# Kernel tuning notes

Hardware: AMD Instinct MI355X
Metric: run time of the kernel (lower is better)

The kernel has to match this reference:

```python
import jax, jax.numpy as jnp
import numpy as np

N_NODES = 100000
N_EDGES = 1600000
IN_CH, HID_CH, OUT_CH = 128, 256, 128


def _sage_conv(x, src, dst, W_l, b_l, W_r, n_nodes):
    """PyG SAGEConv with mean aggregation: lin_l(mean_j x_j) + lin_r(x)."""
    # gather source features per edge, scatter-sum into destination nodes
    agg = jax.ops.segment_sum(x[src], dst, num_segments=n_nodes)  # [N, C]
    deg = jax.ops.segment_sum(jnp.ones((src.shape[0],), x.dtype), dst,
                              num_segments=n_nodes)               # [N]
    mean = agg / jnp.maximum(deg, 1.0)[:, None]
    return mean @ W_l + b_l + x @ W_r


def setup_inputs() -> dict:
    key = jax.random.key(0)
    ks = jax.random.split(key, 8)
    x = jax.random.normal(ks[0], (N_NODES, IN_CH), dtype=jnp.float32)
    edge_index = jax.random.randint(ks[1], (2, N_EDGES), 0, N_NODES, dtype=jnp.int64)
    s1 = 1.0 / np.sqrt(IN_CH)
    s2 = 1.0 / np.sqrt(HID_CH)
    W1_l = jax.random.normal(ks[2], (IN_CH, HID_CH), dtype=jnp.float32) * s1
    W1_r = jax.random.normal(ks[3], (IN_CH, HID_CH), dtype=jnp.float32) * s1
    b1 = jnp.zeros((HID_CH,), dtype=jnp.float32)
    W2_l = jax.random.normal(ks[4], (HID_CH, OUT_CH), dtype=jnp.float32) * s2
    W2_r = jax.random.normal(ks[5], (HID_CH, OUT_CH), dtype=jnp.float32) * s2
    b2 = jnp.zeros((OUT_CH,), dtype=jnp.float32)
    return {"x": x, "edge_index": edge_index, "W1_l": W1_l, "b1": b1,
            "W1_r": W1_r, "W2_l": W2_l, "b2": b2, "W2_r": W2_r}


def reference(x, edge_index, W1_l, b1, W1_r, W2_l, b2, W2_r):
    src, dst = edge_index[0], edge_index[1]
    h = _sage_conv(x, src, dst, W1_l, b1, W1_r, N_NODES)
    h = jax.nn.relu(h)
    out = _sage_conv(h, src, dst, W2_l, b2, W2_r, N_NODES)
    return out
```

## Files before the change

kernel.cpp:

```cpp
#include <hip/hip_runtime.h>
#include <cstddef>

#define N_NODES_C 100000
#define N_EDGES_C 1600000

#define NPB 64
#define NB 1563
#define BCAP 1408
#define SENT_ROW 100000

#define CONV_BLOCKS 12500
#define WB_BLOCKS 512
#define P1_BLOCKS 1563

typedef unsigned short u16;
typedef __attribute__((ext_vector_type(8))) short bf16x8;
typedef __attribute__((ext_vector_type(4))) float f32x4;

__device__ __forceinline__ u16 f2bf(float f) {
    unsigned u = __float_as_uint(f);
    u += 0x7fffu + ((u >> 16) & 1);
    return (u16)(u >> 16);
}
__device__ __forceinline__ float lo16f(unsigned v) {
    return __uint_as_float(v << 16);
}
__device__ __forceinline__ float hi16f(unsigned v) {
    return __uint_as_float(v & 0xffff0000u);
}


__global__ __launch_bounds__(256) void front_fused(
    const float* __restrict__ x, const int* __restrict__ dst,
    const float* __restrict__ W1l, const float* __restrict__ W1r,
    const float* __restrict__ W2l, const float* __restrict__ W2r,
    u16* __restrict__ x_bf, u16* __restrict__ T1l, u16* __restrict__ T1r,
    u16* __restrict__ T2l, u16* __restrict__ T2r,
    int* __restrict__ bucket_counts, u16* __restrict__ p2z) {
    const int b = blockIdx.x;
    const int t = threadIdx.x;
    if (b < CONV_BLOCKS) {
        int i = b * 256 + t;
        if (i < 3200000) {
            float4 v = ((const float4*)x)[i];
            ushort4 o;
            o.x = f2bf(v.x); o.y = f2bf(v.y); o.z = f2bf(v.z); o.w = f2bf(v.w);
            ((ushort4*)x_bf)[i] = o;
        }
    } else if (b < CONV_BLOCKS + WB_BLOCKS) {
        int id = (b - CONV_BLOCKS) * 256 + t;
        int which = id >> 15;
        int r = id & 32767;
        if (which == 0) {
            int n = r >> 7, k = r & 127;
            T1l[r] = f2bf(W1l[k * 256 + n]);
        } else if (which == 1) {
            int n = r >> 7, k = r & 127;
            T1r[r] = f2bf(W1r[k * 256 + n]);
        } else if (which == 2) {
            int n = r >> 8, k = r & 255;
            T2l[r] = f2bf(W2l[k * 128 + n]);
        } else {
            int n = r >> 8, k = r & 255;
            T2r[r] = f2bf(W2r[k * 128 + n]);
        }
    } else if (b < CONV_BLOCKS + WB_BLOCKS + P1_BLOCKS) {
        __shared__ int hist[NB];
        for (int j = t; j < NB; j += 256) hist[j] = 0;
        __syncthreads();
        int i = (b - CONV_BLOCKS - WB_BLOCKS) * 256 + t;
        if (i * 4 < N_EDGES_C) {
            int4 d = ((const int4*)dst)[i];
            atomicAdd(&hist[d.x >> 6], 1);
            atomicAdd(&hist[d.y >> 6], 1);
            atomicAdd(&hist[d.z >> 6], 1);
            atomicAdd(&hist[d.w >> 6], 1);
        }
        __syncthreads();
        for (int j = t; j < NB; j += 256) {
            int c = hist[j];
            if (c) atomicAdd(&bucket_counts[j], c);
        }
    } else {
        uint4 z; z.x = 0; z.y = 0; z.z = 0; z.w = 0;
        if (t < 16)
            ((uint4*)(x_bf + (size_t)SENT_ROW * 128))[t] = z;
        else if (t < 32)
            ((uint4*)(p2z + (size_t)SENT_ROW * 128))[t - 16] = z;
    }
}


__global__ __launch_bounds__(1024) void bucket_scan(const int* __restrict__ counts,
                                                    int* __restrict__ base,
                                                    int* __restrict__ cursor) {
    __shared__ int s[1024];
    int t = threadIdx.x;
    int c0 = counts[2 * t];
    int c1 = counts[2 * t + 1];
    int v = c0 + c1;
    s[t] = v;
    __syncthreads();
    for (int off = 1; off < 1024; off <<= 1) {
        int u = (t >= off) ? s[t - off] : 0;
        __syncthreads();
        s[t] += u;
        __syncthreads();
    }
    int excl = s[t] - v;
    base[2 * t] = excl;
    cursor[2 * t] = excl;
    base[2 * t + 1] = excl + c0;
    cursor[2 * t + 1] = excl + c0;
}


__global__ __launch_bounds__(1024) void p2_scatter(const int* __restrict__ src,
                                                   const int* __restrict__ dst,
                                                   int* __restrict__ cursor,
                                                   unsigned* __restrict__ edge_pkt) {
    __shared__ int hist[NB];
    __shared__ int lbase[NB];
    __shared__ int cur2[NB];
    int t = threadIdx.x;
    for (int j = t; j < NB; j += 1024) { hist[j] = 0; cur2[j] = 0; }
    __syncthreads();

    int4 dd[4];
    int idx[4];
#pragma unroll
    for (int r = 0; r < 4; ++r) {
        int i = blockIdx.x * 4096 + r * 1024 + t;
        idx[r] = i;
        if (i * 4 < N_EDGES_C) {
            int4 d = ((const int4*)dst)[i];
            dd[r] = d;
            atomicAdd(&hist[d.x >> 6], 1);
            atomicAdd(&hist[d.y >> 6], 1);
            atomicAdd(&hist[d.z >> 6], 1);
            atomicAdd(&hist[d.w >> 6], 1);
        }
    }
    __syncthreads();
    for (int j = t; j < NB; j += 1024) {
        int c = hist[j];
        if (c) lbase[j] = atomicAdd(&cursor[j], c);
    }
    __syncthreads();

#pragma unroll
    for (int r = 0; r < 4; ++r) {
        int i = idx[r];
        if (i * 4 < N_EDGES_C) {
            int4 s4 = ((const int4*)src)[i];
            int4 d = dd[r];
            {
                int bk = d.x >> 6, local = d.x & 63;
                int pos = lbase[bk] + atomicAdd(&cur2[bk], 1);
                edge_pkt[pos] = ((unsigned)local << 17) | (unsigned)s4.x;
            }
            {
                int bk = d.y >> 6, local = d.y & 63;
                int pos = lbase[bk] + atomicAdd(&cur2[bk], 1);
                edge_pkt[pos] = ((unsigned)local << 17) | (unsigned)s4.y;
            }
            {
                int bk = d.z >> 6, local = d.z & 63;
                int pos = lbase[bk] + atomicAdd(&cur2[bk], 1);
                edge_pkt[pos] = ((unsigned)local << 17) | (unsigned)s4.z;
            }
            {
                int bk = d.w >> 6, local = d.w & 63;
                int pos = lbase[bk] + atomicAdd(&cur2[bk], 1);
                edge_pkt[pos] = ((unsigned)local << 17) | (unsigned)s4.w;
            }
        }
    }
}


__global__ __launch_bounds__(256, 2) void fused_gemm_agg(
    const u16* __restrict__ x_bf,
    const int* __restrict__ base, const unsigned* __restrict__ edge_pkt,
    const u16* __restrict__ T1l, const u16* __restrict__ T1r,
    const u16* __restrict__ T2l, const u16* __restrict__ T2r,
    const float* __restrict__ b1, const float* __restrict__ b2,
    u16* __restrict__ p2, u16* __restrict__ outp, int M) {
    alignas(16) __shared__ u16 uni[64 * 256];
    alignas(16) __shared__ u16 Bs[8192];
    __shared__ unsigned se[BCAP];
    __shared__ int lhist[64];
    __shared__ int lstart[64];
    __shared__ int lcur[64];
    __shared__ int stmp[64];

    u16* const meanS = uni;
    u16* const xS = uni + 64 * 128;
    u16* const hfrag = uni;

    const int tid = threadIdx.x;
    const int lane = tid & 63;
    const int wave = tid >> 6;
    const int qm = lane & 15;
    const int quad = lane >> 4;
    const int b = blockIdx.x;
    const int m0 = b * 64;

#pragma unroll
    for (int r = 0; r < 4; ++r) {
        int c = r * 256 + tid;
        int row = c >> 4, q16 = c & 15;
        __builtin_amdgcn_global_load_lds(
            (const __attribute__((address_space(1))) unsigned*)(
                x_bf + (size_t)(m0 + row) * 128 + ((q16 ^ (row & 7)) * 8)),
            (__attribute__((address_space(3))) unsigned*)(xS + c * 8), 16, 0, 0);
    }

    if (tid < 64) lhist[tid] = 0;
    __syncthreads();

    const int ebeg = base[b];
    int ecnt = base[b + 1] - ebeg;
    if (ecnt > BCAP) ecnt = BCAP;

    for (int i = tid; i < ecnt; i += 256)
        atomicAdd(&lhist[edge_pkt[ebeg + i] >> 17], 1);
    __syncthreads();

    if (tid < 64) stmp[tid] = lhist[tid];
    __syncthreads();
    for (int off = 1; off < 64; off <<= 1) {
        int v = 0;
        if (tid < 64 && tid >= off) v = stmp[tid - off];
        __syncthreads();
        if (tid < 64) stmp[tid] += v;
        __syncthreads();
    }
    if (tid < 64) {
        int excl = stmp[tid] - lhist[tid];
        lstart[tid] = excl;
        lcur[tid] = excl;
    }
    __syncthreads();

    for (int i = tid; i < ecnt; i += 256) {
        unsigned p = edge_pkt[ebeg + i];
        int pos = atomicAdd(&lcur[p >> 17], 1);
        se[pos] = p & 0x1ffffu;
    }
    __syncthreads();

    const int g = quad;
    const int li16 = qm;
    const int li8 = li16 * 8;

    for (int pass = 0; pass < 4; ++pass) {
        int n = pass * 16 + wave * 4 + g;
        int d = lhist[n];
        int s0 = lstart[n];
        int dmax = max(d, __shfl_xor(d, 16, 64));
        dmax = max(dmax, __shfl_xor(dmax, 32, 64));

        float a0 = 0.f, a1 = 0.f, a2 = 0.f, a3 = 0.f;
        float a4 = 0.f, a5 = 0.f, a6 = 0.f, a7 = 0.f;

        for (int j = 0; j < dmax; j += 4) {
            unsigned ix[4];
#pragma unroll
            for (int u = 0; u < 4; ++u) {
                int jj = j + u;
                int sa = s0 + jj;
                if (sa > BCAP - 1) sa = BCAP - 1;
                unsigned sv = se[sa];
                ix[u] = (jj < d) ? sv : (unsigned)SENT_ROW;
            }
            uint4 r0 = *(const uint4*)(x_bf + (size_t)ix[0] * 128 + li8);
            uint4 r1 = *(const uint4*)(x_bf + (size_t)ix[1] * 128 + li8);
            uint4 r2 = *(const uint4*)(x_bf + (size_t)ix[2] * 128 + li8);
            uint4 r3 = *(const uint4*)(x_bf + (size_t)ix[3] * 128 + li8);

            a0 += lo16f(r0.x); a1 += hi16f(r0.x);
            a2 += lo16f(r0.y); a3 += hi16f(r0.y);
            a4 += lo16f(r0.z); a5 += hi16f(r0.z);
            a6 += lo16f(r0.w); a7 += hi16f(r0.w);
            a0 += lo16f(r1.x); a1 += hi16f(r1.x);
            a2 += lo16f(r1.y); a3 += hi16f(r1.y);
            a4 += lo16f(r1.z); a5 += hi16f(r1.z);
            a6 += lo16f(r1.w); a7 += hi16f(r1.w);
            a0 += lo16f(r2.x); a1 += hi16f(r2.x);
            a2 += lo16f(r2.y); a3 += hi16f(r2.y);
            a4 += lo16f(r2.z); a5 += hi16f(r2.z);
            a6 += lo16f(r2.w); a7 += hi16f(r2.w);
            a0 += lo16f(r3.x); a1 += hi16f(r3.x);
            a2 += lo16f(r3.y); a3 += hi16f(r3.y);
            a4 += lo16f(r3.z); a5 += hi16f(r3.z);
            a6 += lo16f(r3.w); a7 += hi16f(r3.w);
        }

        float inv = d > 0 ? 1.f / (float)d : 0.f;
        uint4 o;
        o.x = (unsigned)f2bf(a0 * inv) | ((unsigned)f2bf(a1 * inv) << 16);
        o.y = (unsigned)f2bf(a2 * inv) | ((unsigned)f2bf(a3 * inv) << 16);
        o.z = (unsigned)f2bf(a4 * inv) | ((unsigned)f2bf(a5 * inv) << 16);
        o.w = (unsigned)f2bf(a6 * inv) | ((unsigned)f2bf(a7 * inv) << 16);
        *(uint4*)(meanS + n * 128 + ((li16 ^ (n & 7)) * 8)) = o;
    }
    __syncthreads();

    const int wr0 = (wave >> 1) * 32;
    const int wc0 = (wave & 1) * 128;
    f32x4 acch[2][8];
#pragma unroll
    for (int i = 0; i < 2; ++i)
#pragma unroll
        for (int j = 0; j < 8; ++j) acch[i][j] = (f32x4){0.f, 0.f, 0.f, 0.f};

#pragma unroll
    for (int mat = 0; mat < 2; ++mat) {
        const u16* __restrict__ W = mat ? T1r : T1l;
        const u16* Al = mat ? xS : meanS;
#pragma unroll
        for (int k0 = 0; k0 < 128; k0 += 32) {
#pragma unroll
            for (int r = 0; r < 4; ++r) {
                int c = r * 256 + tid;
                int row = c >> 2, kc = c & 3;
                __builtin_amdgcn_global_load_lds(
                    (const __attribute__((address_space(1))) unsigned*)(
                        W + (size_t)row * 128 + k0 + ((kc ^ (row & 3)) * 8)),
                    (__attribute__((address_space(3))) unsigned*)(Bs + c * 8), 16, 0, 0);
            }
            __syncthreads();
            int ch0 = k0 >> 3;
            bf16x8 af[2], bfv[8];
#pragma unroll
            for (int i = 0; i < 2; ++i) {
                int row = wr0 + i * 16 + qm;
                af[i] = *(const bf16x8*)(Al + row * 128 +
                                         (((ch0 + quad) ^ (row & 7)) * 8));
            }
#pragma unroll
            for (int j = 0; j < 8; ++j) {
                int rB = wc0 + j * 16 + qm;
                bfv[j] = *(const bf16x8*)(Bs + rB * 32 + ((quad ^ (rB & 3)) * 8));
            }
#pragma unroll
            for (int i = 0; i < 2; ++i)
#pragma unroll
                for (int j = 0; j < 8; ++j)
                    acch[i][j] = __builtin_amdgcn_mfma_f32_16x16x32_bf16(
                        af[i], bfv[j], acch[i][j], 0, 0, 0);
            __syncthreads();
        }
    }

#pragma unroll
    for (int j = 0; j < 8; ++j) {
        int n = wc0 + j * 16 + qm;
        float bb = b1[n];
        int ks = n >> 5, quadB = (n >> 3) & 3, jB = n & 7;
#pragma unroll
        for (int i = 0; i < 2; ++i) {
#pragma unroll
            for (int r = 0; r < 4; ++r) {
                int mloc = wr0 + i * 16 + quad * 4 + r;
                float v = fmaxf(acch[i][j][r] + bb, 0.f);
                hfrag[((ks * 4 + (mloc >> 4)) * 16 + (mloc & 15)) * 32 + quadB * 8 + jB] =
                    f2bf(v);
            }
        }
    }
    __syncthreads();

    const int wrB = (wave >> 1) * 32;
    const int wcB = (wave & 1) * 64;
    f32x4 accp[2][4], acco[2][4];
#pragma unroll
    for (int i = 0; i < 2; ++i)
#pragma unroll
        for (int j = 0; j < 4; ++j) {
            accp[i][j] = (f32x4){0.f, 0.f, 0.f, 0.f};
            acco[i][j] = (f32x4){0.f, 0.f, 0.f, 0.f};
        }

#pragma unroll
    for (int ks = 0; ks < 8; ++ks) {
#pragma unroll
        for (int r = 0; r < 4; ++r) {
            int c = r * 256 + tid;
            int matc = c >> 9;
            int row = (c >> 2) & 127;
            int kc = c & 3;
            const u16* W = matc ? T2r : T2l;
            __builtin_amdgcn_global_load_lds(
                (const __attribute__((address_space(1))) unsigned*)(
                    W + (size_t)row * 256 + ks * 32 + ((kc ^ (row & 3)) * 8)),
                (__attribute__((address_space(3))) unsigned*)(Bs + c * 8), 16, 0, 0);
        }
        __syncthreads();
        bf16x8 af[2], bfl[4], bfr[4];
#pragma unroll
        for (int i = 0; i < 2; ++i)
            af[i] = *(const bf16x8*)(hfrag +
                                     ((ks * 4 + (wrB >> 4) + i) * 16 + qm) * 32 + quad * 8);
#pragma unroll
        for (int j = 0; j < 4; ++j) {
            int rB = wcB + j * 16 + qm;
            bfl[j] = *(const bf16x8*)(Bs + rB * 32 + ((quad ^ (rB & 3)) * 8));
            bfr[j] = *(const bf16x8*)(Bs + 4096 + rB * 32 + ((quad ^ (rB & 3)) * 8));
        }
#pragma unroll
        for (int i = 0; i < 2; ++i)
#pragma unroll
            for (int j = 0; j < 4; ++j) {
                accp[i][j] = __builtin_amdgcn_mfma_f32_16x16x32_bf16(af[i], bfl[j],
                                                                    accp[i][j], 0, 0, 0);
                acco[i][j] = __builtin_amdgcn_mfma_f32_16x16x32_bf16(af[i], bfr[j],
                                                                    acco[i][j], 0, 0, 0);
            }
        __syncthreads();
    }

#pragma unroll
    for (int j = 0; j < 4; ++j) {
        int n = wcB + j * 16 + qm;
        float bb2 = b2[n];
#pragma unroll
        for (int i = 0; i < 2; ++i) {
#pragma unroll
            for (int r = 0; r < 4; ++r) {
                int row = m0 + wrB + i * 16 + quad * 4 + r;
                if (row < M) {
                    p2[(size_t)row * 128 + n] = f2bf(accp[i][j][r]);
                    outp[(size_t)row * 128 + n] = f2bf(acco[i][j][r] + bb2);
                }
            }
        }
    }
}


__global__ __launch_bounds__(256, 8) void agg_final(const u16* __restrict__ tbl,
                                                    const int* __restrict__ base,
                                                    const unsigned* __restrict__ edge_pkt,
                                                    const u16* __restrict__ resid,
                                                    float* __restrict__ outv) {
    __shared__ unsigned se[BCAP];
    __shared__ int lhist[64];
    __shared__ int lstart[64];
    __shared__ int lcur[64];
    __shared__ int stmp[64];

    const int t = threadIdx.x;
    const int wave = t >> 6;
    const int lane = t & 63;
    const int b = blockIdx.x;

    if (t < 64) lhist[t] = 0;
    __syncthreads();

    const int ebeg = base[b];
    int ecnt = base[b + 1] - ebeg;
    if (ecnt > BCAP) ecnt = BCAP;

    for (int i = t; i < ecnt; i += 256)
        atomicAdd(&lhist[edge_pkt[ebeg + i] >> 17], 1);
    __syncthreads();

    if (t < 64) stmp[t] = lhist[t];
    __syncthreads();
    for (int off = 1; off < 64; off <<= 1) {
        int v = 0;
        if (t < 64 && t >= off) v = stmp[t - off];
        __syncthreads();
        if (t < 64) stmp[t] += v;
        __syncthreads();
    }
    if (t < 64) {
        int excl = stmp[t] - lhist[t];
        lstart[t] = excl;
        lcur[t] = excl;
    }
    __syncthreads();

    for (int i = t; i < ecnt; i += 256) {
        unsigned p = edge_pkt[ebeg + i];
        int pos = atomicAdd(&lcur[p >> 17], 1);
        se[pos] = p & 0x1ffffu;
    }
    __syncthreads();

    const int g = lane >> 4;
    const int li8 = (lane & 15) * 8;

    for (int pass = 0; pass < 4; ++pass) {
        int n = pass * 16 + wave * 4 + g;
        int node = b * NPB + n;
        bool valid = node < N_NODES_C;
        int d = 0, s0 = 0;
        if (valid) { d = lhist[n]; s0 = lstart[n]; }
        int dmax = max(d, __shfl_xor(d, 16, 64));
        dmax = max(dmax, __shfl_xor(dmax, 32, 64));

        float a0 = 0.f, a1 = 0.f, a2 = 0.f, a3 = 0.f;
        float a4 = 0.f, a5 = 0.f, a6 = 0.f, a7 = 0.f;

        for (int j = 0; j < dmax; j += 4) {
            unsigned ix[4];
#pragma unroll
            for (int u = 0; u < 4; ++u) {
                int jj = j + u;
                int sa = s0 + jj;
                if (sa > BCAP - 1) sa = BCAP - 1;
                unsigned sv = se[sa];
                ix[u] = (jj < d) ? sv : (unsigned)SENT_ROW;
            }
            uint4 r0 = *(const uint4*)(tbl + (size_t)ix[0] * 128 + li8);
            uint4 r1 = *(const uint4*)(tbl + (size_t)ix[1] * 128 + li8);
            uint4 r2 = *(const uint4*)(tbl + (size_t)ix[2] * 128 + li8);
            uint4 r3 = *(const uint4*)(tbl + (size_t)ix[3] * 128 + li8);

            a0 += lo16f(r0.x); a1 += hi16f(r0.x);
            a2 += lo16f(r0.y); a3 += hi16f(r0.y);
            a4 += lo16f(r0.z); a5 += hi16f(r0.z);
            a6 += lo16f(r0.w); a7 += hi16f(r0.w);
            a0 += lo16f(r1.x); a1 += hi16f(r1.x);
            a2 += lo16f(r1.y); a3 += hi16f(r1.y);
            a4 += lo16f(r1.z); a5 += hi16f(r1.z);
            a6 += lo16f(r1.w); a7 += hi16f(r1.w);
            a0 += lo16f(r2.x); a1 += hi16f(r2.x);
            a2 += lo16f(r2.y); a3 += hi16f(r2.y);
            a4 += lo16f(r2.z); a5 += hi16f(r2.z);
            a6 += lo16f(r2.w); a7 += hi16f(r2.w);
            a0 += lo16f(r3.x); a1 += hi16f(r3.x);
            a2 += lo16f(r3.y); a3 += hi16f(r3.y);
            a4 += lo16f(r3.z); a5 += hi16f(r3.z);
            a6 += lo16f(r3.w); a7 += hi16f(r3.w);
        }

        if (valid) {
            float inv = d > 0 ? 1.f / (float)d : 0.f;
            uint4 rp = *(const uint4*)(resid + (size_t)node * 128 + li8);
            float* op = outv + (size_t)node * 128 + li8;
            float4 o0, o1;
            o0.x = a0 * inv + lo16f(rp.x);
            o0.y = a1 * inv + hi16f(rp.x);
            o0.z = a2 * inv + lo16f(rp.y);
            o0.w = a3 * inv + hi16f(rp.y);
            o1.x = a4 * inv + lo16f(rp.z);
            o1.y = a5 * inv + hi16f(rp.z);
            o1.z = a6 * inv + lo16f(rp.w);
            o1.w = a7 * inv + hi16f(rp.w);
            *(float4*)op = o0;
            *(float4*)(op + 4) = o1;
        }
    }
}


extern "C" void kernel_launch(void* const* d_in, const int* in_sizes, int n_in,
                              void* d_out, int out_size, void* d_ws, size_t ws_size,
                              hipStream_t stream) {
    const float* x = (const float*)d_in[0];
    const int* ei = (const int*)d_in[1];
    const float* W1l = (const float*)d_in[2];
    const float* b1 = (const float*)d_in[3];
    const float* W1r = (const float*)d_in[4];
    const float* W2l = (const float*)d_in[5];
    const float* b2 = (const float*)d_in[6];
    const float* W2r = (const float*)d_in[7];
    float* out = (float*)d_out;

    const int* src = ei;
    const int* dst = ei + N_EDGES_C;

    int* iw = (int*)d_ws;
    int* bucket_counts = iw;
    int* bucket_base = iw + 2048;
    int* cursor = iw + 4096;
    unsigned* edge_pkt = (unsigned*)(iw + 6144);
    u16* T1l = (u16*)(iw + 1606144);
    u16* T1r = T1l + 32768;
    u16* T2l = T1r + 32768;
    u16* T2r = T2l + 32768;
    u16* ub = (u16*)((char*)d_ws + (8u << 20));
    u16* x_bf = ub;
    u16* p2 = ub + 12850000;
    u16* outp = ub + 25700000;

    hipMemsetAsync(bucket_counts, 0, 2048 * sizeof(int), stream);

    front_fused<<<CONV_BLOCKS + WB_BLOCKS + P1_BLOCKS + 1, 256, 0, stream>>>(
        x, dst, W1l, W1r, W2l, W2r, x_bf, T1l, T1r, T2l, T2r, bucket_counts, p2);
    bucket_scan<<<1, 1024, 0, stream>>>(bucket_counts, bucket_base, cursor);
    p2_scatter<<<(N_EDGES_C / 4 + 4095) / 4096, 1024, 0, stream>>>(src, dst, cursor,
                                                                   edge_pkt);

    fused_gemm_agg<<<NB, 256, 0, stream>>>(x_bf, bucket_base, edge_pkt, T1l, T1r,
                                           T2l, T2r, b1, b2, p2, outp, N_NODES_C);
    agg_final<<<NB, 256, 0, stream>>>(p2, bucket_base, edge_pkt, outp, out);
}
```

Baseline: 396.9 us.

## Build per-node CSR with global atomics and drop per-block LDS edge sort

Replaces the bucketed edge packing and in-kernel LDS counting sort with a per-node degree histogram, a multi-block scan with atomic offset allocation, and direct per-node scatter of source indices. The aggregation loops read indices from global memory, coalesced per 16 lanes, and broadcast them with shuffles. The fused GEMM kernel is widened to 512 threads with smaller per-wave tiles. This removes LDS sort and barrier overhead and the edge-capacity cap, at the price of many more contended global atomics in the degree and scatter passes.

```diff
diff --git a/kernel.cpp b/kernel.cpp
--- a/kernel.cpp
+++ b/kernel.cpp
@@ -6,12 +6,11 @@
 
 #define NPB 64
 #define NB 1563
-#define BCAP 1408
 #define SENT_ROW 100000
 
 #define CONV_BLOCKS 12500
 #define WB_BLOCKS 512
-#define P1_BLOCKS 1563
+#define DEG_BLOCKS 1563
 
 typedef unsigned short u16;
 typedef __attribute__((ext_vector_type(8))) short bf16x8;
@@ -36,7 +35,7 @@
     const float* __restrict__ W2l, const float* __restrict__ W2r,
     u16* __restrict__ x_bf, u16* __restrict__ T1l, u16* __restrict__ T1r,
     u16* __restrict__ T2l, u16* __restrict__ T2r,
-    int* __restrict__ bucket_counts, u16* __restrict__ p2z) {
+    int* __restrict__ deg, u16* __restrict__ p2z) {
     const int b = blockIdx.x;
     const int t = threadIdx.x;
     if (b < CONV_BLOCKS) {
@@ -64,22 +63,14 @@
             int n = r >> 8, k = r & 255;
             T2r[r] = f2bf(W2r[k * 128 + n]);
         }
-    } else if (b < CONV_BLOCKS + WB_BLOCKS + P1_BLOCKS) {
-        __shared__ int hist[NB];
-        for (int j = t; j < NB; j += 256) hist[j] = 0;
-        __syncthreads();
+    } else if (b < CONV_BLOCKS + WB_BLOCKS + DEG_BLOCKS) {
         int i = (b - CONV_BLOCKS - WB_BLOCKS) * 256 + t;
         if (i * 4 < N_EDGES_C) {
             int4 d = ((const int4*)dst)[i];
-            atomicAdd(&hist[d.x >> 6], 1);
-            atomicAdd(&hist[d.y >> 6], 1);
-            atomicAdd(&hist[d.z >> 6], 1);
-            atomicAdd(&hist[d.w >> 6], 1);
-        }
-        __syncthreads();
-        for (int j = t; j < NB; j += 256) {
-            int c = hist[j];
-            if (c) atomicAdd(&bucket_counts[j], c);
+            atomicAdd(&deg[d.x], 1);
+            atomicAdd(&deg[d.y], 1);
+            atomicAdd(&deg[d.z], 1);
+            atomicAdd(&deg[d.w], 1);
         }
     } else {
         uint4 z; z.x = 0; z.y = 0; z.z = 0; z.w = 0;
@@ -91,14 +82,15 @@
 }
 
 
-__global__ __launch_bounds__(1024) void bucket_scan(const int* __restrict__ counts,
-                                                    int* __restrict__ base,
-                                                    int* __restrict__ cursor) {
+__global__ __launch_bounds__(1024) void scan_alloc(const int* __restrict__ deg,
+                                                   int* __restrict__ gctr,
+                                                   int* __restrict__ base,
+                                                   int* __restrict__ cursor) {
     __shared__ int s[1024];
+    __shared__ int sofs;
     int t = threadIdx.x;
-    int c0 = counts[2 * t];
-    int c1 = counts[2 * t + 1];
-    int v = c0 + c1;
+    int i = blockIdx.x * 1024 + t;
+    int v = (i < N_NODES_C) ? deg[i] : 0;
     s[t] = v;
     __syncthreads();
     for (int off = 1; off < 1024; off <<= 1) {
@@ -107,92 +99,41 @@
         s[t] += u;
         __syncthreads();
     }
-    int excl = s[t] - v;
-    base[2 * t] = excl;
-    cursor[2 * t] = excl;
-    base[2 * t + 1] = excl + c0;
-    cursor[2 * t + 1] = excl + c0;
+    if (t == 1023) sofs = atomicAdd(gctr, s[1023]);
+    __syncthreads();
+    if (i < N_NODES_C) {
+        int e = sofs + s[t] - v;
+        base[i] = e;
+        cursor[i] = e;
+    }
 }
 
 
 __global__ __launch_bounds__(1024) void p2_scatter(const int* __restrict__ src,
                                                    const int* __restrict__ dst,
                                                    int* __restrict__ cursor,
-                                                   unsigned* __restrict__ edge_pkt) {
-    __shared__ int hist[NB];
-    __shared__ int lbase[NB];
-    __shared__ int cur2[NB];
-    int t = threadIdx.x;
-    for (int j = t; j < NB; j += 1024) { hist[j] = 0; cur2[j] = 0; }
-    __syncthreads();
-
-    int4 dd[4];
-    int idx[4];
-#pragma unroll
-    for (int r = 0; r < 4; ++r) {
-        int i = blockIdx.x * 4096 + r * 1024 + t;
-        idx[r] = i;
-        if (i * 4 < N_EDGES_C) {
-            int4 d = ((const int4*)dst)[i];
-            dd[r] = d;
-            atomicAdd(&hist[d.x >> 6], 1);
-            atomicAdd(&hist[d.y >> 6], 1);
-            atomicAdd(&hist[d.z >> 6], 1);
-            atomicAdd(&hist[d.w >> 6], 1);
-        }
-    }
-    __syncthreads();
-    for (int j = t; j < NB; j += 1024) {
-        int c = hist[j];
-        if (c) lbase[j] = atomicAdd(&cursor[j], c);
-    }
-    __syncthreads();
-
-#pragma unroll
-    for (int r = 0; r < 4; ++r) {
-        int i = idx[r];
-        if (i * 4 < N_EDGES_C) {
-            int4 s4 = ((const int4*)src)[i];
-            int4 d = dd[r];
-            {
-                int bk = d.x >> 6, local = d.x & 63;
-                int pos = lbase[bk] + atomicAdd(&cur2[bk], 1);
-                edge_pkt[pos] = ((unsigned)local << 17) | (unsigned)s4.x;
-            }
-            {
-                int bk = d.y >> 6, local = d.y & 63;
-                int pos = lbase[bk] + atomicAdd(&cur2[bk], 1);
-                edge_pkt[pos] = ((unsigned)local << 17) | (unsigned)s4.y;
-            }
-            {
-                int bk = d.z >> 6, local = d.z & 63;
-                int pos = lbase[bk] + atomicAdd(&cur2[bk], 1);
-                edge_pkt[pos] = ((unsigned)local << 17) | (unsigned)s4.z;
-            }
-            {
-                int bk = d.w >> 6, local = d.w & 63;
-                int pos = lbase[bk] + atomicAdd(&cur2[bk], 1);
-                edge_pkt[pos] = ((unsigned)local << 17) | (unsigned)s4.w;
-            }
-        }
-    }
-}
-
-
-__global__ __launch_bounds__(256, 2) void fused_gemm_agg(
-    const u16* __restrict__ x_bf,
-    const int* __restrict__ base, const unsigned* __restrict__ edge_pkt,
+                                                   unsigned* __restrict__ esrc) {
+    int i = blockIdx.x * 1024 + threadIdx.x;
+    if (i * 4 >= N_EDGES_C) return;
+    int4 d = ((const int4*)dst)[i];
+    int4 s4 = ((const int4*)src)[i];
+    int p;
+    p = atomicAdd(&cursor[d.x], 1); esrc[p] = (unsigned)s4.x;
+    p = atomicAdd(&cursor[d.y], 1); esrc[p] = (unsigned)s4.y;
+    p = atomicAdd(&cursor[d.z], 1); esrc[p] = (unsigned)s4.z;
+    p = atomicAdd(&cursor[d.w], 1); esrc[p] = (unsigned)s4.w;
+}
+
+
+__global__ __launch_bounds__(512, 6) void fused_gemm_agg(
+    const u16* __restrict__ x_bf, const int* __restrict__ deg,
+    const int* __restrict__ base, const unsigned* __restrict__ esrc,
     const u16* __restrict__ T1l, const u16* __restrict__ T1r,
     const u16* __restrict__ T2l, const u16* __restrict__ T2r,
     const float* __restrict__ b1, const float* __restrict__ b2,
     u16* __restrict__ p2, u16* __restrict__ outp, int M) {
     alignas(16) __shared__ u16 uni[64 * 256];
     alignas(16) __shared__ u16 Bs[8192];
-    __shared__ unsigned se[BCAP];
-    __shared__ int lhist[64];
-    __shared__ int lstart[64];
-    __shared__ int lcur[64];
-    __shared__ int stmp[64];
 
     u16* const meanS = uni;
     u16* const xS = uni + 64 * 128;
@@ -207,8 +148,8 @@
     const int m0 = b * 64;
 
 #pragma unroll
-    for (int r = 0; r < 4; ++r) {
-        int c = r * 256 + tid;
+    for (int r = 0; r < 2; ++r) {
+        int c = r * 512 + tid;
         int row = c >> 4, q16 = c & 15;
         __builtin_amdgcn_global_load_lds(
             (const __attribute__((address_space(1))) unsigned*)(
@@ -216,85 +157,49 @@
             (__attribute__((address_space(3))) unsigned*)(xS + c * 8), 16, 0, 0);
     }
 
-    if (tid < 64) lhist[tid] = 0;
-    __syncthreads();
-
-    const int ebeg = base[b];
-    int ecnt = base[b + 1] - ebeg;
-    if (ecnt > BCAP) ecnt = BCAP;
-
-    for (int i = tid; i < ecnt; i += 256)
-        atomicAdd(&lhist[edge_pkt[ebeg + i] >> 17], 1);
-    __syncthreads();
-
-    if (tid < 64) stmp[tid] = lhist[tid];
-    __syncthreads();
-    for (int off = 1; off < 64; off <<= 1) {
-        int v = 0;
-        if (tid < 64 && tid >= off) v = stmp[tid - off];
-        __syncthreads();
-        if (tid < 64) stmp[tid] += v;
-        __syncthreads();
-    }
-    if (tid < 64) {
-        int excl = stmp[tid] - lhist[tid];
-        lstart[tid] = excl;
-        lcur[tid] = excl;
-    }
-    __syncthreads();
-
-    for (int i = tid; i < ecnt; i += 256) {
-        unsigned p = edge_pkt[ebeg + i];
-        int pos = atomicAdd(&lcur[p >> 17], 1);
-        se[pos] = p & 0x1ffffu;
-    }
-    __syncthreads();
-
-    const int g = quad;
-    const int li16 = qm;
-    const int li8 = li16 * 8;
-
-    for (int pass = 0; pass < 4; ++pass) {
-        int n = pass * 16 + wave * 4 + g;
-        int d = lhist[n];
-        int s0 = lstart[n];
+    const int li8 = qm * 8;
+    const int gbase = lane & 48;
+
+    for (int pass = 0; pass < 2; ++pass) {
+        int n = pass * 32 + wave * 4 + quad;
+        int node = m0 + n;
+        int d = 0, s0 = 0;
+        if (node < N_NODES_C) { d = deg[node]; s0 = base[node]; }
         int dmax = max(d, __shfl_xor(d, 16, 64));
         dmax = max(dmax, __shfl_xor(dmax, 32, 64));
 
         float a0 = 0.f, a1 = 0.f, a2 = 0.f, a3 = 0.f;
         float a4 = 0.f, a5 = 0.f, a6 = 0.f, a7 = 0.f;
 
-        for (int j = 0; j < dmax; j += 4) {
-            unsigned ix[4];
-#pragma unroll
-            for (int u = 0; u < 4; ++u) {
-                int jj = j + u;
-                int sa = s0 + jj;
-                if (sa > BCAP - 1) sa = BCAP - 1;
-                unsigned sv = se[sa];
-                ix[u] = (jj < d) ? sv : (unsigned)SENT_ROW;
+        for (int j = 0; j < dmax; j += 16) {
+            int jj = j + qm;
+            unsigned sidx = (jj < d) ? esrc[s0 + jj] : (unsigned)SENT_ROW;
+            for (int u = 0; u < 16 && j + u < dmax; u += 4) {
+                unsigned i0 = __shfl(sidx, gbase + u, 64);
+                unsigned i1 = __shfl(sidx, gbase + u + 1, 64);
+                unsigned i2 = __shfl(sidx, gbase + u + 2, 64);
+                unsigned i3 = __shfl(sidx, gbase + u + 3, 64);
+                uint4 r0 = *(const uint4*)(x_bf + (size_t)i0 * 128 + li8);
+                uint4 r1 = *(const uint4*)(x_bf + (size_t)i1 * 128 + li8);
+                uint4 r2 = *(const uint4*)(x_bf + (size_t)i2 * 128 + li8);
+                uint4 r3 = *(const uint4*)(x_bf + (size_t)i3 * 128 + li8);
+                a0 += lo16f(r0.x); a1 += hi16f(r0.x);
+                a2 += lo16f(r0.y); a3 += hi16f(r0.y);
+                a4 += lo16f(r0.z); a5 += hi16f(r0.z);
+                a6 += lo16f(r0.w); a7 += hi16f(r0.w);
+                a0 += lo16f(r1.x); a1 += hi16f(r1.x);
+                a2 += lo16f(r1.y); a3 += hi16f(r1.y);
+                a4 += lo16f(r1.z); a5 += hi16f(r1.z);
+                a6 += lo16f(r1.w); a7 += hi16f(r1.w);
+                a0 += lo16f(r2.x); a1 += hi16f(r2.x);
+                a2 += lo16f(r2.y); a3 += hi16f(r2.y);
+                a4 += lo16f(r2.z); a5 += hi16f(r2.z);
+                a6 += lo16f(r2.w); a7 += hi16f(r2.w);
+                a0 += lo16f(r3.x); a1 += hi16f(r3.x);
+                a2 += lo16f(r3.y); a3 += hi16f(r3.y);
+                a4 += lo16f(r3.z); a5 += hi16f(r3.z);
+                a6 += lo16f(r3.w); a7 += hi16f(r3.w);
             }
-            uint4 r0 = *(const uint4*)(x_bf + (size_t)ix[0] * 128 + li8);
-            uint4 r1 = *(const uint4*)(x_bf + (size_t)ix[1] * 128 + li8);
-            uint4 r2 = *(const uint4*)(x_bf + (size_t)ix[2] * 128 + li8);
-            uint4 r3 = *(const uint4*)(x_bf + (size_t)ix[3] * 128 + li8);
-
-            a0 += lo16f(r0.x); a1 += hi16f(r0.x);
-            a2 += lo16f(r0.y); a3 += hi16f(r0.y);
-            a4 += lo16f(r0.z); a5 += hi16f(r0.z);
-            a6 += lo16f(r0.w); a7 += hi16f(r0.w);
-            a0 += lo16f(r1.x); a1 += hi16f(r1.x);
-            a2 += lo16f(r1.y); a3 += hi16f(r1.y);
-            a4 += lo16f(r1.z); a5 += hi16f(r1.z);
-            a6 += lo16f(r1.w); a7 += hi16f(r1.w);
-            a0 += lo16f(r2.x); a1 += hi16f(r2.x);
-            a2 += lo16f(r2.y); a3 += hi16f(r2.y);
-            a4 += lo16f(r2.z); a5 += hi16f(r2.z);
-            a6 += lo16f(r2.w); a7 += hi16f(r2.w);
-            a0 += lo16f(r3.x); a1 += hi16f(r3.x);
-            a2 += lo16f(r3.y); a3 += hi16f(r3.y);
-            a4 += lo16f(r3.z); a5 += hi16f(r3.z);
-            a6 += lo16f(r3.w); a7 += hi16f(r3.w);
         }
 
         float inv = d > 0 ? 1.f / (float)d : 0.f;
@@ -303,17 +208,15 @@
         o.y = (unsigned)f2bf(a2 * inv) | ((unsigned)f2bf(a3 * inv) << 16);
         o.z = (unsigned)f2bf(a4 * inv) | ((unsigned)f2bf(a5 * inv) << 16);
         o.w = (unsigned)f2bf(a6 * inv) | ((unsigned)f2bf(a7 * inv) << 16);
-        *(uint4*)(meanS + n * 128 + ((li16 ^ (n & 7)) * 8)) = o;
+        *(uint4*)(meanS + n * 128 + ((qm ^ (n & 7)) * 8)) = o;
     }
     __syncthreads();
 
-    const int wr0 = (wave >> 1) * 32;
+    const int wr0 = (wave >> 1) * 16;
     const int wc0 = (wave & 1) * 128;
-    f32x4 acch[2][8];
-#pragma unroll
-    for (int i = 0; i < 2; ++i)
-#pragma unroll
-        for (int j = 0; j < 8; ++j) acch[i][j] = (f32x4){0.f, 0.f, 0.f, 0.f};
+    f32x4 acch[8];
+#pragma unroll
+    for (int j = 0; j < 8; ++j) acch[j] = (f32x4){0.f, 0.f, 0.f, 0.f};
 
 #pragma unroll
     for (int mat = 0; mat < 2; ++mat) {
@@ -322,8 +225,8 @@
 #pragma unroll
         for (int k0 = 0; k0 < 128; k0 += 32) {
 #pragma unroll
-            for (int r = 0; r < 4; ++r) {
-                int c = r * 256 + tid;
+            for (int r = 0; r < 2; ++r) {
+                int c = r * 512 + tid;
                 int row = c >> 2, kc = c & 3;
                 __builtin_amdgcn_global_load_lds(
                     (const __attribute__((address_space(1))) unsigned*)(
@@ -332,24 +235,19 @@
             }
             __syncthreads();
             int ch0 = k0 >> 3;
-            bf16x8 af[2], bfv[8];
-#pragma unroll
-            for (int i = 0; i < 2; ++i) {
-                int row = wr0 + i * 16 + qm;
-                af[i] = *(const bf16x8*)(Al + row * 128 +
-                                         (((ch0 + quad) ^ (row & 7)) * 8));
-            }
+            int rowA = wr0 + qm;
+            bf16x8 af = *(const bf16x8*)(Al + rowA * 128 +
+                                         (((ch0 + quad) ^ (rowA & 7)) * 8));
+            bf16x8 bfv[8];
 #pragma unroll
             for (int j = 0; j < 8; ++j) {
                 int rB = wc0 + j * 16 + qm;
                 bfv[j] = *(const bf16x8*)(Bs + rB * 32 + ((quad ^ (rB & 3)) * 8));
             }
 #pragma unroll
-            for (int i = 0; i < 2; ++i)
-#pragma unroll
-                for (int j = 0; j < 8; ++j)
-                    acch[i][j] = __builtin_amdgcn_mfma_f32_16x16x32_bf16(
-                        af[i], bfv[j], acch[i][j], 0, 0, 0);
+            for (int j = 0; j < 8; ++j)
+                acch[j] = __builtin_amdgcn_mfma_f32_16x16x32_bf16(af, bfv[j],
+                                                                  acch[j], 0, 0, 0);
             __syncthreads();
         }
     }
@@ -360,34 +258,29 @@
         float bb = b1[n];
         int ks = n >> 5, quadB = (n >> 3) & 3, jB = n & 7;
 #pragma unroll
-        for (int i = 0; i < 2; ++i) {
-#pragma unroll
-            for (int r = 0; r < 4; ++r) {
-                int mloc = wr0 + i * 16 + quad * 4 + r;
-                float v = fmaxf(acch[i][j][r] + bb, 0.f);
-                hfrag[((ks * 4 + (mloc >> 4)) * 16 + (mloc & 15)) * 32 + quadB * 8 + jB] =
-                    f2bf(v);
-            }
+        for (int r = 0; r < 4; ++r) {
+            int mloc = wr0 + quad * 4 + r;
+            float v = fmaxf(acch[j][r] + bb, 0.f);
+            hfrag[((ks * 4 + (mloc >> 4)) * 16 + (mloc & 15)) * 32 + quadB * 8 + jB] =
+                f2bf(v);
         }
     }
     __syncthreads();
 
-    const int wrB = (wave >> 1) * 32;
+    const int wrB = (wave >> 1) * 16;
     const int wcB = (wave & 1) * 64;
-    f32x4 accp[2][4], acco[2][4];
-#pragma unroll
-    for (int i = 0; i < 2; ++i)
-#pragma unroll
-        for (int j = 0; j < 4; ++j) {
-            accp[i][j] = (f32x4){0.f, 0.f, 0.f, 0.f};
-            acco[i][j] = (f32x4){0.f, 0.f, 0.f, 0.f};
-        }
+    f32x4 accp[4], acco[4];
+#pragma unroll
+    for (int j = 0; j < 4; ++j) {
+        accp[j] = (f32x4){0.f, 0.f, 0.f, 0.f};
+        acco[j] = (f32x4){0.f, 0.f, 0.f, 0.f};
+    }
 
 #pragma unroll
     for (int ks = 0; ks < 8; ++ks) {
 #pragma unroll
-        for (int r = 0; r < 4; ++r) {
-            int c = r * 256 + tid;
+        for (int r = 0; r < 2; ++r) {
+            int c = r * 512 + tid;
             int matc = c >> 9;
             int row = (c >> 2) & 127;
             int kc = c & 3;
@@ -398,11 +291,9 @@
                 (__attribute__((address_space(3))) unsigned*)(Bs + c * 8), 16, 0, 0);
         }
         __syncthreads();
-        bf16x8 af[2], bfl[4], bfr[4];
-#pragma unroll
-        for (int i = 0; i < 2; ++i)
-            af[i] = *(const bf16x8*)(hfrag +
-                                     ((ks * 4 + (wrB >> 4) + i) * 16 + qm) * 32 + quad * 8);
+        bf16x8 af = *(const bf16x8*)(hfrag +
+                                     ((ks * 4 + (wrB >> 4)) * 16 + qm) * 32 + quad * 8);
+        bf16x8 bfl[4], bfr[4];
 #pragma unroll
         for (int j = 0; j < 4; ++j) {
             int rB = wcB + j * 16 + qm;
@@ -410,14 +301,12 @@
             bfr[j] = *(const bf16x8*)(Bs + 4096 + rB * 32 + ((quad ^ (rB & 3)) * 8));
         }
 #pragma unroll
-        for (int i = 0; i < 2; ++i)
-#pragma unroll
-            for (int j = 0; j < 4; ++j) {
-                accp[i][j] = __builtin_amdgcn_mfma_f32_16x16x32_bf16(af[i], bfl[j],
-                                                                    accp[i][j], 0, 0, 0);
-                acco[i][j] = __builtin_amdgcn_mfma_f32_16x16x32_bf16(af[i], bfr[j],
-                                                                    acco[i][j], 0, 0, 0);
-            }
+        for (int j = 0; j < 4; ++j) {
+            accp[j] = __builtin_amdgcn_mfma_f32_16x16x32_bf16(af, bfl[j],
+                                                              accp[j], 0, 0, 0);
+            acco[j] = __builtin_amdgcn_mfma_f32_16x16x32_bf16(af, bfr[j],
+                                                              acco[j], 0, 0, 0);
+        }
         __syncthreads();
     }
 
@@ -426,14 +315,11 @@
         int n = wcB + j * 16 + qm;
         float bb2 = b2[n];
 #pragma unroll
-        for (int i = 0; i < 2; ++i) {
-#pragma unroll
-            for (int r = 0; r < 4; ++r) {
-                int row = m0 + wrB + i * 16 + quad * 4 + r;
-                if (row < M) {
-                    p2[(size_t)row * 128 + n] = f2bf(accp[i][j][r]);
-                    outp[(size_t)row * 128 + n] = f2bf(acco[i][j][r] + bb2);
-                }
+        for (int r = 0; r < 4; ++r) {
+            int row = m0 + wrB + quad * 4 + r;
+            if (row < M) {
+                p2[(size_t)row * 128 + n] = f2bf(accp[j][r]);
+                outp[(size_t)row * 128 + n] = f2bf(acco[j][r] + bb2);
             }
         }
     }
@@ -441,101 +327,61 @@
 
 
 __global__ __launch_bounds__(256, 8) void agg_final(const u16* __restrict__ tbl,
+                                                    const int* __restrict__ deg,
                                                     const int* __restrict__ base,
-                                                    const unsigned* __restrict__ edge_pkt,
+                                                    const unsigned* __restrict__ esrc,
                                                     const u16* __restrict__ resid,
                                                     float* __restrict__ outv) {
-    __shared__ unsigned se[BCAP];
-    __shared__ int lhist[64];
-    __shared__ int lstart[64];
-    __shared__ int lcur[64];
-    __shared__ int stmp[64];
-
     const int t = threadIdx.x;
     const int wave = t >> 6;
     const int lane = t & 63;
+    const int qm = lane & 15;
+    const int quad = lane >> 4;
     const int b = blockIdx.x;
-
-    if (t < 64) lhist[t] = 0;
-    __syncthreads();
-
-    const int ebeg = base[b];
-    int ecnt = base[b + 1] - ebeg;
-    if (ecnt > BCAP) ecnt = BCAP;
-
-    for (int i = t; i < ecnt; i += 256)
-        atomicAdd(&lhist[edge_pkt[ebeg + i] >> 17], 1);
-    __syncthreads();
-
-    if (t < 64) stmp[t] = lhist[t];
-    __syncthreads();
-    for (int off = 1; off < 64; off <<= 1) {
-        int v = 0;
-        if (t < 64 && t >= off) v = stmp[t - off];
-        __syncthreads();
-        if (t < 64) stmp[t] += v;
-        __syncthreads();
-    }
-    if (t < 64) {
-        int excl = stmp[t] - lhist[t];
-        lstart[t] = excl;
-        lcur[t] = excl;
-    }
-    __syncthreads();
-
-    for (int i = t; i < ecnt; i += 256) {
-        unsigned p = edge_pkt[ebeg + i];
-        int pos = atomicAdd(&lcur[p >> 17], 1);
-        se[pos] = p & 0x1ffffu;
-    }
-    __syncthreads();
-
-    const int g = lane >> 4;
-    const int li8 = (lane & 15) * 8;
+    const int li8 = qm * 8;
+    const int gbase = lane & 48;
 
     for (int pass = 0; pass < 4; ++pass) {
-        int n = pass * 16 + wave * 4 + g;
+        int n = pass * 16 + wave * 4 + quad;
         int node = b * NPB + n;
         bool valid = node < N_NODES_C;
         int d = 0, s0 = 0;
-        if (valid) { d = lhist[n]; s0 = lstart[n]; }
+        if (valid) { d = deg[node]; s0 = base[node]; }
         int dmax = max(d, __shfl_xor(d, 16, 64));
         dmax = max(dmax, __shfl_xor(dmax, 32, 64));
 
         float a0 = 0.f, a1 = 0.f, a2 = 0.f, a3 = 0.f;
         float a4 = 0.f, a5 = 0.f, a6 = 0.f, a7 = 0.f;
 
-        for (int j = 0; j < dmax; j += 4) {
-            unsigned ix[4];
-#pragma unroll
-            for (int u = 0; u < 4; ++u) {
-                int jj = j + u;
-                int sa = s0 + jj;
-                if (sa > BCAP - 1) sa = BCAP - 1;
-                unsigned sv = se[sa];
-                ix[u] = (jj < d) ? sv : (unsigned)SENT_ROW;
+        for (int j = 0; j < dmax; j += 16) {
+            int jj = j + qm;
+            unsigned sidx = (jj < d) ? esrc[s0 + jj] : (unsigned)SENT_ROW;
+            for (int u = 0; u < 16 && j + u < dmax; u += 4) {
+                unsigned i0 = __shfl(sidx, gbase + u, 64);
+                unsigned i1 = __shfl(sidx, gbase + u + 1, 64);
+                unsigned i2 = __shfl(sidx, gbase + u + 2, 64);
+                unsigned i3 = __shfl(sidx, gbase + u + 3, 64);
+                uint4 r0 = *(const uint4*)(tbl + (size_t)i0 * 128 + li8);
+                uint4 r1 = *(const uint4*)(tbl + (size_t)i1 * 128 + li8);
+                uint4 r2 = *(const uint4*)(tbl + (size_t)i2 * 128 + li8);
+                uint4 r3 = *(const uint4*)(tbl + (size_t)i3 * 128 + li8);
+                a0 += lo16f(r0.x); a1 += hi16f(r0.x);
+                a2 += lo16f(r0.y); a3 += hi16f(r0.y);
+                a4 += lo16f(r0.z); a5 += hi16f(r0.z);
+                a6 += lo16f(r0.w); a7 += hi16f(r0.w);
+                a0 += lo16f(r1.x); a1 += hi16f(r1.x);
+                a2 += lo16f(r1.y); a3 += hi16f(r1.y);
+                a4 += lo16f(r1.z); a5 += hi16f(r1.z);
+                a6 += lo16f(r1.w); a7 += hi16f(r1.w);
+                a0 += lo16f(r2.x); a1 += hi16f(r2.x);
+                a2 += lo16f(r2.y); a3 += hi16f(r2.y);
+                a4 += lo16f(r2.z); a5 += hi16f(r2.z);
+                a6 += lo16f(r2.w); a7 += hi16f(r2.w);
+                a0 += lo16f(r3.x); a1 += hi16f(r3.x);
+                a2 += lo16f(r3.y); a3 += hi16f(r3.y);
+                a4 += lo16f(r3.z); a5 += hi16f(r3.z);
+                a6 += lo16f(r3.w); a7 += hi16f(r3.w);
             }
-            uint4 r0 = *(const uint4*)(tbl + (size_t)ix[0] * 128 + li8);
-            uint4 r1 = *(const uint4*)(tbl + (size_t)ix[1] * 128 + li8);
-            uint4 r2 = *(const uint4*)(tbl + (size_t)ix[2] * 128 + li8);
-            uint4 r3 = *(const uint4*)(tbl + (size_t)ix[3] * 128 + li8);
-
-            a0 += lo16f(r0.x); a1 += hi16f(r0.x);
-            a2 += lo16f(r0.y); a3 += hi16f(r0.y);
-            a4 += lo16f(r0.z); a5 += hi16f(r0.z);
-            a6 += lo16f(r0.w); a7 += hi16f(r0.w);
-            a0 += lo16f(r1.x); a1 += hi16f(r1.x);
-            a2 += lo16f(r1.y); a3 += hi16f(r1.y);
-            a4 += lo16f(r1.z); a5 += hi16f(r1.z);
-            a6 += lo16f(r1.w); a7 += hi16f(r1.w);
-            a0 += lo16f(r2.x); a1 += hi16f(r2.x);
-            a2 += lo16f(r2.y); a3 += hi16f(r2.y);
-            a4 += lo16f(r2.z); a5 += hi16f(r2.z);
-            a6 += lo16f(r2.w); a7 += hi16f(r2.w);
-            a0 += lo16f(r3.x); a1 += hi16f(r3.x);
-            a2 += lo16f(r3.y); a3 += hi16f(r3.y);
-            a4 += lo16f(r3.z); a5 += hi16f(r3.z);
-            a6 += lo16f(r3.w); a7 += hi16f(r3.w);
         }
 
         if (valid) {
@@ -575,11 +421,12 @@
     const int* dst = ei + N_EDGES_C;
 
     int* iw = (int*)d_ws;
-    int* bucket_counts = iw;
-    int* bucket_base = iw + 2048;
-    int* cursor = iw + 4096;
-    unsigned* edge_pkt = (unsigned*)(iw + 6144);
-    u16* T1l = (u16*)(iw + 1606144);
+    int* deg = iw;
+    int* gctr = iw + 100000;
+    int* base = iw + 100352;
+    int* cursor = iw + 200704;
+    unsigned* esrc = (unsigned*)(iw + 301056);
+    u16* T1l = (u16*)(iw + 1901568);
     u16* T1r = T1l + 32768;
     u16* T2l = T1r + 32768;
     u16* T2r = T2l + 32768;
@@ -588,15 +435,15 @@
     u16* p2 = ub + 12850000;
     u16* outp = ub + 25700000;
 
-    hipMemsetAsync(bucket_counts, 0, 2048 * sizeof(int), stream);
-
-    front_fused<<<CONV_BLOCKS + WB_BLOCKS + P1_BLOCKS + 1, 256, 0, stream>>>(
-        x, dst, W1l, W1r, W2l, W2r, x_bf, T1l, T1r, T2l, T2r, bucket_counts, p2);
-    bucket_scan<<<1, 1024, 0, stream>>>(bucket_counts, bucket_base, cursor);
-    p2_scatter<<<(N_EDGES_C / 4 + 4095) / 4096, 1024, 0, stream>>>(src, dst, cursor,
-                                                                   edge_pkt);
-
-    fused_gemm_agg<<<NB, 256, 0, stream>>>(x_bf, bucket_base, edge_pkt, T1l, T1r,
-                                           T2l, T2r, b1, b2, p2, outp, N_NODES_C);
-    agg_final<<<NB, 256, 0, stream>>>(p2, bucket_base, edge_pkt, outp, out);
-}
+    hipMemsetAsync(deg, 0, 100001 * sizeof(int), stream);
+
+    front_fused<<<CONV_BLOCKS + WB_BLOCKS + DEG_BLOCKS + 1, 256, 0, stream>>>(
+        x, dst, W1l, W1r, W2l, W2r, x_bf, T1l, T1r, T2l, T2r, deg, p2);
+    scan_alloc<<<98, 1024, 0, stream>>>(deg, gctr, base, cursor);
+    p2_scatter<<<(N_EDGES_C / 4 + 1023) / 1024, 1024, 0, stream>>>(src, dst, cursor,
+                                                                   esrc);
+
+    fused_gemm_agg<<<NB, 512, 0, stream>>>(x_bf, deg, base, esrc, T1l, T1r, T2l,
+                                           T2r, b1, b2, p2, outp, N_NODES_C);
+    agg_final<<<NB, 256, 0, stream>>>(p2, deg, base, esrc, outp, out);
+}
```

Result: slower. 479.8 us (+20.9%).
